# Optimization experiments

Hardware: AMD Instinct MI355X
Metric: run time of the kernel (lower is better)

The kernel has to match this reference:

```python
import jax, jax.numpy as jnp
import numpy as np

N_GAS_NETS = 76  # 29 h2o + 13 o3 + 9 co2 + 3 n2o + 9 ch4 + 13 uniform
N_CHANNELS = 29
N_IN = 2   # (temperature, pressure)
H = 64     # hidden width per n_hidden=[64,64]

# gas index (into composition[0..5]) for each of the 76 stacked nets
COMP_IDX = jnp.asarray(np.repeat(np.arange(6), [29, 13, 9, 3, 9, 13]))

# sparse per-channel combine (hard-coded in the original forward)
H2O_IDX = jnp.asarray([0,1,2,3,4,5,6,3,4,9,10,11,12,13,14,15,16,17,18,19,20,21,22,23,24,25,26,27,28])
O3_CH  = jnp.asarray([0,1,2,17,18,19,20,21,22,25,26,27,28])
CO2_CH = jnp.asarray([0,1,2,5,6,9,10,13,14])
N2O_CH = jnp.asarray([0,1,2])
CH4_CH = jnp.asarray([0,1,2,3,4,7,8,11,12])
U_CH   = jnp.asarray([0,1,2,15,16,17,18,19,20,21,22,27,28])


def setup_inputs() -> dict:
    key = jax.random.key(0)
    ks = jax.random.split(key, 10)
    N = 32768
    t_p = jax.random.normal(ks[0], (N, N_IN), dtype=jnp.float32)
    composition = jax.random.uniform(ks[1], (8, N, 1), dtype=jnp.float32)
    s1 = 1.0 / np.sqrt(N_IN)
    s2 = 1.0 / np.sqrt(H)
    W1 = jax.random.normal(ks[2], (N_GAS_NETS, N_IN, H), dtype=jnp.float32) * s1
    b1 = jnp.zeros((N_GAS_NETS, H), dtype=jnp.float32)
    W2 = jax.random.normal(ks[3], (N_GAS_NETS, H, H), dtype=jnp.float32) * s2
    b2 = jnp.zeros((N_GAS_NETS, H), dtype=jnp.float32)
    Wout = jax.random.normal(ks[4], (N_GAS_NETS, H, 1), dtype=jnp.float32) * s2
    bout = jnp.zeros((N_GAS_NETS, 1), dtype=jnp.float32)
    ke_lw = jax.random.uniform(ks[5], (N_CHANNELS, 1), dtype=jnp.float32)
    ke_iw = jax.random.uniform(ks[6], (N_CHANNELS, 1), dtype=jnp.float32)
    return {"t_p": t_p, "composition": composition, "W1": W1, "b1": b1,
            "W2": W2, "b2": b2, "Wout": Wout, "bout": bout,
            "ke_lw": ke_lw, "ke_iw": ke_iw}


def reference(t_p, composition, W1, b1, W2, b2, Wout, bout, ke_lw, ke_iw):
    # Batched evaluation of all 76 tiny DenseFFN experts on the shared t_p input.
    h = jax.nn.relu(jnp.einsum('ni,gih->gnh', t_p, W1) + b1[:, None, :])   # [76,N,H]
    h = jax.nn.relu(jnp.einsum('gnh,ghk->gnk', h, W2) + b2[:, None, :])    # [76,N,H]
    ke = jax.nn.relu(jnp.einsum('gnh,gho->gno', h, Wout) + bout[:, None, :])  # [76,N,1]

    # tau_gas[gas] = ke * composition[gas_index]
    tau_all = ke * composition[COMP_IDX]  # [76,N,1]
    h2o = tau_all[0:29]
    o3 = tau_all[29:42]
    co2 = tau_all[42:51]
    n2o = tau_all[51:54]
    ch4 = tau_all[54:63]
    u = tau_all[63:76]

    # hard-coded sparse per-channel sum
    tau_gases = h2o[H2O_IDX]                      # [29,N,1]
    tau_gases = tau_gases.at[O3_CH].add(o3)
    tau_gases = tau_gases.at[CO2_CH].add(co2)
    tau_gases = tau_gases.at[N2O_CH].add(n2o)
    tau_gases = tau_gases.at[CH4_CH].add(ch4)
    tau_gases = tau_gases.at[U_CH].add(u)

    tau_lw = ke_lw[:, None, :] * composition[6]   # [29,N,1]
    tau_iw = ke_iw[:, None, :] * composition[7]   # [29,N,1]
    return (tau_gases, tau_lw, tau_iw)
```

## Files before the change

kernel.cpp:

```cpp
#include <hip/hip_runtime.h>

#define NPTS 32768

typedef _Float16 f16;
typedef _Float16 f16x2 __attribute__((ext_vector_type(2)));
typedef _Float16 f16x8 __attribute__((ext_vector_type(8)));
typedef float f32x2 __attribute__((ext_vector_type(2)));
typedef float f32x4 __attribute__((ext_vector_type(4)));
typedef unsigned int u32x4 __attribute__((ext_vector_type(4)));

union U16 { u32x4 u; f32x4 f; f16x2 h2[4]; f16x8 h8; };

static __device__ __forceinline__ f16x2 pk_fma(f16x2 a, f16x2 b, f16x2 c) {
  return __builtin_elementwise_fma(a, b, c);
}
static __device__ __forceinline__ f16x2 pk_relu(f16x2 a) {
  f16x2 z = {(f16)0.f, (f16)0.f};
  return __builtin_elementwise_max(a, z);
}
static __device__ __forceinline__ f16x2 pk_cvt(float a, float b) {
  return __builtin_bit_cast(f16x2, __builtin_amdgcn_cvt_pkrtz(a, b));
}

__device__ const unsigned char G_T[74] = {
  0,0,0,0,0,0,0, 0,0,0,0,0,0,0,0,0,0,0,0,0,0,0,0,0,0,0,0,
  1,1,1,1,1,1,1,1,1,1,1,1,1,
  2,2,2,2,2,2,2,2,2,
  3,3,3,
  4,4,4,4,4,4,4,4,4,
  5,5,5,5,5,5,5,5,5,5,5,5,5
};
__device__ const unsigned char G_C1[74] = {
  0,1,2,3,4,5,6, 9,10,11,12,13,14,15,16,17,18,19,20,21,22,23,24,25,26,27,28,
  0,1,2,17,18,19,20,21,22,25,26,27,28,
  0,1,2,5,6,9,10,13,14,
  0,1,2,
  0,1,2,3,4,7,8,11,12,
  0,1,2,15,16,17,18,19,20,21,22,27,28
};
__device__ const unsigned char G_C2[74] = {
  255,255,255,7,8,255,255, 255,255,255,255,255,255,255,255,255,255,255,255,
  255,255,255,255,255,255,255,255,
  255,255,255,255,255,255,255,255,255,255,255,255,255,
  255,255,255,255,255,255,255,255,255,
  255,255,255,
  255,255,255,255,255,255,255,255,255,
  255,255,255,255,255,255,255,255,255,255,255,255,255
};

#define NSLOT 22

__global__ __launch_bounds__(64) void k0w_pack(
    const float* __restrict__ W1, const float* __restrict__ b1,
    const float* __restrict__ W2, const float* __restrict__ b2,
    const float* __restrict__ Wout, u32x4* __restrict__ pack)
{
  const int gi   = blockIdx.x;
  const int lane = threadIdx.x;
  const int l15  = lane & 15;
  const int quad = lane >> 4;
  const int g    = gi + (gi >= 7 ? 2 : 0);

  const float* W2g = W2 + g * 4096;
  const float* W1g = W1 + g * 128;
  const float* b1g = b1 + g * 64;
  u32x4* dst = pack + gi * NSLOT * 64 + lane;

  #pragma unroll
  for (int mt = 0; mt < 4; ++mt)
    #pragma unroll
    for (int ks = 0; ks < 2; ++ks) {
      U16 u;
      #pragma unroll
      for (int j = 0; j < 4; ++j) {
        const float* s = W2g + (ks * 32 + quad * 8 + 2 * j) * 64 + mt * 16 + l15;
        u.h2[j] = pk_cvt(s[0], s[64]);
      }
      dst[(mt * 2 + ks) * 64] = u.u;
    }
  #pragma unroll
  for (int ks = 0; ks < 2; ++ks) {
    U16 a, b, c;
    #pragma unroll
    for (int j = 0; j < 4; ++j) {
      int h = ks * 32 + quad * 8 + 2 * j;
      a.h2[j] = pk_cvt(W1g[h],      W1g[h + 1]);
      b.h2[j] = pk_cvt(W1g[64 + h], W1g[64 + h + 1]);
      c.h2[j] = pk_cvt(b1g[h],      b1g[h + 1]);
    }
    dst[(8 + ks) * 64]  = a.u;
    dst[(10 + ks) * 64] = b.u;
    dst[(12 + ks) * 64] = c.u;
  }
  #pragma unroll
  for (int mt = 0; mt < 4; ++mt) {
    U16 u, v;
    u.f = *(const f32x4*)(b2   + g * 64 + mt * 16 + quad * 4);
    v.f = *(const f32x4*)(Wout + g * 64 + mt * 16 + quad * 4);
    dst[(14 + mt) * 64] = u.u;
    dst[(18 + mt) * 64] = v.u;
  }
}

__global__ __launch_bounds__(256) void k0_init(
    const float* __restrict__ comp, const float* __restrict__ ke_lw,
    const float* __restrict__ ke_iw, float* __restrict__ out)
{
  const int c = blockIdx.x >> 7;
  const int n = ((blockIdx.x & 127) << 8) + threadIdx.x;
  out[c * NPTS + n] = 0.f;
  out[29 * NPTS + c * NPTS + n] = ke_lw[c] * comp[6 * NPTS + n];
  out[58 * NPTS + c * NPTS + n] = ke_iw[c] * comp[7 * NPTS + n];
}

__global__ __launch_bounds__(256, 2) void k1_mlp(
    const float* __restrict__ t_p, const float* __restrict__ comp,
    const u32x4* __restrict__ pack, const float* __restrict__ bout,
    float* __restrict__ out)
{
  const int lane = threadIdx.x & 63;
  const int l15  = lane & 15;
  const int quad = lane >> 4;
  const int w    = blockIdx.x * 4 + (threadIdx.x >> 6);
  const int gi   = w >> 6;
  const int g    = gi + (gi >= 7 ? 2 : 0);
  const int pb0  = (w & 63) * 512;

  const int t  = G_T[gi];
  const int c1 = G_C1[gi];
  const int c2 = G_C2[gi];

  const bool qb0 = (quad & 1) != 0;
  const bool qb1 = (quad & 2) != 0;

  const u32x4* pksrc = pack + gi * NSLOT * 64 + lane;
  f16x8 afrag[4][2];
  f32x4 b2q[4];
  f32x2 wq2[4][2];
  #pragma unroll
  for (int mt = 0; mt < 4; ++mt) {
    afrag[mt][0] = __builtin_bit_cast(f16x8, pksrc[(mt * 2 + 0) * 64]);
    afrag[mt][1] = __builtin_bit_cast(f16x8, pksrc[(mt * 2 + 1) * 64]);
    b2q[mt] = __builtin_bit_cast(f32x4, pksrc[(14 + mt) * 64]);
    f32x4 wv = __builtin_bit_cast(f32x4, pksrc[(18 + mt) * 64]);
    wq2[mt][0] = f32x2{ wv[0], wv[1] };
    wq2[mt][1] = f32x2{ wv[2], wv[3] };
  }
  U16 w0s[2], w1s[2], b1s[2];
  #pragma unroll
  for (int ks = 0; ks < 2; ++ks) {
    w0s[ks].u = pksrc[(8 + ks) * 64];
    w1s[ks].u = pksrc[(10 + ks) * 64];
    b1s[ks].u = pksrc[(12 + ks) * 64];
  }
  const float bo = bout[g];

  const float2* tp2 = (const float2*)t_p;
  const float* compt = comp + t * NPTS;
  float* out1 = out + c1 * NPTS;
  float* out2 = (c2 == 255) ? nullptr : out + c2 * NPTS;

  for (int pass = 0; pass < 8; ++pass) {
    const int pb = pb0 + pass * 64;

    float2 xv[4];
    #pragma unroll
    for (int pt = 0; pt < 4; ++pt)
      xv[pt] = tp2[pb + pt * 16 + l15];
    const float cv = compt[pb + lane];

    f16x2 x0v[4], x1v[4];
    #pragma unroll
    for (int pt = 0; pt < 4; ++pt) {
      x0v[pt] = pk_cvt(xv[pt].x, xv[pt].x);
      x1v[pt] = pk_cvt(xv[pt].y, xv[pt].y);
    }

    U16 bfrag[2][4];
    #pragma unroll
    for (int ks = 0; ks < 2; ++ks)
      #pragma unroll
      for (int pt = 0; pt < 4; ++pt)
        #pragma unroll
        for (int i = 0; i < 4; ++i)
          bfrag[ks][pt].h2[i] =
              pk_relu(pk_fma(x0v[pt], w0s[ks].h2[i],
                             pk_fma(x1v[pt], w1s[ks].h2[i], b1s[ks].h2[i])));

    f32x2 p2[4];
    #pragma unroll
    for (int pt = 0; pt < 4; ++pt) p2[pt] = f32x2{ 0.f, 0.f };

    #pragma unroll
    for (int mt = 0; mt < 4; ++mt) {
      f32x4 c[4];
      #pragma unroll
      for (int pt = 0; pt < 4; ++pt)
        c[pt] = __builtin_amdgcn_mfma_f32_16x16x32_f16(
            afrag[mt][0], bfrag[0][pt].h8, b2q[mt], 0, 0, 0);
      #pragma unroll
      for (int pt = 0; pt < 4; ++pt)
        c[pt] = __builtin_amdgcn_mfma_f32_16x16x32_f16(
            afrag[mt][1], bfrag[1][pt].h8, c[pt], 0, 0, 0);
      #pragma unroll
      for (int pt = 0; pt < 4; ++pt) {
        f32x2 z = { 0.f, 0.f };
        f32x2 a0 = { c[pt][0], c[pt][1] };
        f32x2 a1 = { c[pt][2], c[pt][3] };
        a0 = __builtin_elementwise_max(a0, z);
        a1 = __builtin_elementwise_max(a1, z);
        p2[pt] = __builtin_elementwise_fma(a0, wq2[mt][0], p2[pt]);
        p2[pt] = __builtin_elementwise_fma(a1, wq2[mt][1], p2[pt]);
      }
    }

    float p[4];
    #pragma unroll
    for (int pt = 0; pt < 4; ++pt) p[pt] = p2[pt][0] + p2[pt][1];

    float u  = qb1 ? (qb0 ? p[3] : p[2]) : (qb0 ? p[1] : p[0]);
    float v  = qb1 ? (qb0 ? p[2] : p[3]) : (qb0 ? p[0] : p[1]);
    float w2 = qb1 ? (qb0 ? p[1] : p[0]) : (qb0 ? p[3] : p[2]);
    float x  = qb1 ? (qb0 ? p[0] : p[1]) : (qb0 ? p[2] : p[3]);
    float s  = u + __shfl_xor(v, 16, 64);
    float tt = w2 + __shfl_xor(x, 16, 64);
    float r  = s + __shfl_xor(tt, 32, 64);

    float tau = fmaxf(r + bo, 0.f) * cv;
    atomicAdd(&out1[pb + lane], tau);
    if (out2) atomicAdd(&out2[pb + lane], tau);
  }
}

extern "C" void kernel_launch(void* const* d_in, const int* in_sizes, int n_in,
                              void* d_out, int out_size, void* d_ws, size_t ws_size,
                              hipStream_t stream)
{
  const float* t_p   = (const float*)d_in[0];
  const float* comp  = (const float*)d_in[1];
  const float* W1    = (const float*)d_in[2];
  const float* b1    = (const float*)d_in[3];
  const float* W2    = (const float*)d_in[4];
  const float* b2    = (const float*)d_in[5];
  const float* Wout  = (const float*)d_in[6];
  const float* bout  = (const float*)d_in[7];
  const float* ke_lw = (const float*)d_in[8];
  const float* ke_iw = (const float*)d_in[9];
  float* out = (float*)d_out;
  u32x4* pack = (u32x4*)d_ws;

  k0w_pack<<<74, 64, 0, stream>>>(W1, b1, W2, b2, Wout, pack);
  k0_init<<<29 * 128, 256, 0, stream>>>(comp, ke_lw, ke_iw, out);
  k1_mlp<<<1184, 256, 0, stream>>>(t_p, comp, pack, bout, out);
}
```

Measured before the change: 113.6 us.

## Balance MLP work across a fixed persistent grid with contiguous unit ranges

Replaces the fixed mapping of one wave per (net, 512-point chunk) with a persistent-style grid of 512 blocks. Each wave takes a contiguous range of 64-point units across nets and reloads net weights whenever it crosses a net boundary. This spreads the 74×512 units evenly over all waves to reduce tail imbalance. It also drops the min-2-blocks launch bound and launches through the cooperative API, falling back to a normal launch on error, which adds host overhead and occasional weight reloads in exchange.

```diff
diff --git a/kernel.cpp b/kernel.cpp
--- a/kernel.cpp
+++ b/kernel.cpp
@@ -113,7 +113,7 @@
   out[58 * NPTS + c * NPTS + n] = ke_iw[c] * comp[7 * NPTS + n];
 }
 
-__global__ __launch_bounds__(256, 2) void k1_mlp(
+__global__ __launch_bounds__(256) void k1_mlp(
     const float* __restrict__ t_p, const float* __restrict__ comp,
     const u32x4* __restrict__ pack, const float* __restrict__ bout,
     float* __restrict__ out)
@@ -121,114 +121,122 @@
   const int lane = threadIdx.x & 63;
   const int l15  = lane & 15;
   const int quad = lane >> 4;
-  const int w    = blockIdx.x * 4 + (threadIdx.x >> 6);
-  const int gi   = w >> 6;
-  const int g    = gi + (gi >= 7 ? 2 : 0);
-  const int pb0  = (w & 63) * 512;
-
-  const int t  = G_T[gi];
-  const int c1 = G_C1[gi];
-  const int c2 = G_C2[gi];
+  const int wv   = blockIdx.x * 4 + (threadIdx.x >> 6);
+  const int NW   = gridDim.x * 4;
+  const int TOT  = 74 * 512;
+
+  int u        = (int)(((long long)wv * TOT) / NW);
+  const int u1 = (int)(((long long)(wv + 1) * TOT) / NW);
 
   const bool qb0 = (quad & 1) != 0;
   const bool qb1 = (quad & 2) != 0;
 
-  const u32x4* pksrc = pack + gi * NSLOT * 64 + lane;
-  f16x8 afrag[4][2];
-  f32x4 b2q[4];
-  f32x2 wq2[4][2];
-  #pragma unroll
-  for (int mt = 0; mt < 4; ++mt) {
-    afrag[mt][0] = __builtin_bit_cast(f16x8, pksrc[(mt * 2 + 0) * 64]);
-    afrag[mt][1] = __builtin_bit_cast(f16x8, pksrc[(mt * 2 + 1) * 64]);
-    b2q[mt] = __builtin_bit_cast(f32x4, pksrc[(14 + mt) * 64]);
-    f32x4 wv = __builtin_bit_cast(f32x4, pksrc[(18 + mt) * 64]);
-    wq2[mt][0] = f32x2{ wv[0], wv[1] };
-    wq2[mt][1] = f32x2{ wv[2], wv[3] };
-  }
-  U16 w0s[2], w1s[2], b1s[2];
-  #pragma unroll
-  for (int ks = 0; ks < 2; ++ks) {
-    w0s[ks].u = pksrc[(8 + ks) * 64];
-    w1s[ks].u = pksrc[(10 + ks) * 64];
-    b1s[ks].u = pksrc[(12 + ks) * 64];
-  }
-  const float bo = bout[g];
-
   const float2* tp2 = (const float2*)t_p;
-  const float* compt = comp + t * NPTS;
-  float* out1 = out + c1 * NPTS;
-  float* out2 = (c2 == 255) ? nullptr : out + c2 * NPTS;
-
-  for (int pass = 0; pass < 8; ++pass) {
-    const int pb = pb0 + pass * 64;
-
-    float2 xv[4];
-    #pragma unroll
-    for (int pt = 0; pt < 4; ++pt)
-      xv[pt] = tp2[pb + pt * 16 + l15];
-    const float cv = compt[pb + lane];
-
-    f16x2 x0v[4], x1v[4];
-    #pragma unroll
-    for (int pt = 0; pt < 4; ++pt) {
-      x0v[pt] = pk_cvt(xv[pt].x, xv[pt].x);
-      x1v[pt] = pk_cvt(xv[pt].y, xv[pt].y);
-    }
-
-    U16 bfrag[2][4];
-    #pragma unroll
-    for (int ks = 0; ks < 2; ++ks)
+
+  while (u < u1) {
+    const int gi   = u >> 9;
+    const int uend = min(u1, (gi + 1) << 9);
+    const int g    = gi + (gi >= 7 ? 2 : 0);
+
+    const int t  = G_T[gi];
+    const int c1 = G_C1[gi];
+    const int c2 = G_C2[gi];
+
+    const u32x4* pksrc = pack + gi * NSLOT * 64 + lane;
+    f16x8 afrag[4][2];
+    f32x4 b2q[4];
+    f32x2 wq2[4][2];
+    #pragma unroll
+    for (int mt = 0; mt < 4; ++mt) {
+      afrag[mt][0] = __builtin_bit_cast(f16x8, pksrc[(mt * 2 + 0) * 64]);
+      afrag[mt][1] = __builtin_bit_cast(f16x8, pksrc[(mt * 2 + 1) * 64]);
+      b2q[mt] = __builtin_bit_cast(f32x4, pksrc[(14 + mt) * 64]);
+      f32x4 wvv = __builtin_bit_cast(f32x4, pksrc[(18 + mt) * 64]);
+      wq2[mt][0] = f32x2{ wvv[0], wvv[1] };
+      wq2[mt][1] = f32x2{ wvv[2], wvv[3] };
+    }
+    U16 w0s[2], w1s[2], b1s[2];
+    #pragma unroll
+    for (int ks = 0; ks < 2; ++ks) {
+      w0s[ks].u = pksrc[(8 + ks) * 64];
+      w1s[ks].u = pksrc[(10 + ks) * 64];
+      b1s[ks].u = pksrc[(12 + ks) * 64];
+    }
+    const float bo = bout[g];
+    const float* compt = comp + t * NPTS;
+    float* out1 = out + c1 * NPTS;
+    float* out2 = (c2 == 255) ? nullptr : out + c2 * NPTS;
+
+    for (; u < uend; ++u) {
+      const int pb = (u & 511) * 64;
+
+      float2 xv[4];
       #pragma unroll
       for (int pt = 0; pt < 4; ++pt)
-        #pragma unroll
-        for (int i = 0; i < 4; ++i)
-          bfrag[ks][pt].h2[i] =
-              pk_relu(pk_fma(x0v[pt], w0s[ks].h2[i],
-                             pk_fma(x1v[pt], w1s[ks].h2[i], b1s[ks].h2[i])));
-
-    f32x2 p2[4];
-    #pragma unroll
-    for (int pt = 0; pt < 4; ++pt) p2[pt] = f32x2{ 0.f, 0.f };
-
-    #pragma unroll
-    for (int mt = 0; mt < 4; ++mt) {
-      f32x4 c[4];
-      #pragma unroll
-      for (int pt = 0; pt < 4; ++pt)
-        c[pt] = __builtin_amdgcn_mfma_f32_16x16x32_f16(
-            afrag[mt][0], bfrag[0][pt].h8, b2q[mt], 0, 0, 0);
-      #pragma unroll
-      for (int pt = 0; pt < 4; ++pt)
-        c[pt] = __builtin_amdgcn_mfma_f32_16x16x32_f16(
-            afrag[mt][1], bfrag[1][pt].h8, c[pt], 0, 0, 0);
+        xv[pt] = tp2[pb + pt * 16 + l15];
+      const float cv = compt[pb + lane];
+
+      f16x2 x0v[4], x1v[4];
       #pragma unroll
       for (int pt = 0; pt < 4; ++pt) {
-        f32x2 z = { 0.f, 0.f };
-        f32x2 a0 = { c[pt][0], c[pt][1] };
-        f32x2 a1 = { c[pt][2], c[pt][3] };
-        a0 = __builtin_elementwise_max(a0, z);
-        a1 = __builtin_elementwise_max(a1, z);
-        p2[pt] = __builtin_elementwise_fma(a0, wq2[mt][0], p2[pt]);
-        p2[pt] = __builtin_elementwise_fma(a1, wq2[mt][1], p2[pt]);
+        x0v[pt] = pk_cvt(xv[pt].x, xv[pt].x);
+        x1v[pt] = pk_cvt(xv[pt].y, xv[pt].y);
       }
-    }
-
-    float p[4];
-    #pragma unroll
-    for (int pt = 0; pt < 4; ++pt) p[pt] = p2[pt][0] + p2[pt][1];
-
-    float u  = qb1 ? (qb0 ? p[3] : p[2]) : (qb0 ? p[1] : p[0]);
-    float v  = qb1 ? (qb0 ? p[2] : p[3]) : (qb0 ? p[0] : p[1]);
-    float w2 = qb1 ? (qb0 ? p[1] : p[0]) : (qb0 ? p[3] : p[2]);
-    float x  = qb1 ? (qb0 ? p[0] : p[1]) : (qb0 ? p[2] : p[3]);
-    float s  = u + __shfl_xor(v, 16, 64);
-    float tt = w2 + __shfl_xor(x, 16, 64);
-    float r  = s + __shfl_xor(tt, 32, 64);
-
-    float tau = fmaxf(r + bo, 0.f) * cv;
-    atomicAdd(&out1[pb + lane], tau);
-    if (out2) atomicAdd(&out2[pb + lane], tau);
+
+      U16 bfrag[2][4];
+      #pragma unroll
+      for (int ks = 0; ks < 2; ++ks)
+        #pragma unroll
+        for (int pt = 0; pt < 4; ++pt)
+          #pragma unroll
+          for (int i = 0; i < 4; ++i)
+            bfrag[ks][pt].h2[i] =
+                pk_relu(pk_fma(x0v[pt], w0s[ks].h2[i],
+                               pk_fma(x1v[pt], w1s[ks].h2[i], b1s[ks].h2[i])));
+
+      f32x2 p2[4];
+      #pragma unroll
+      for (int pt = 0; pt < 4; ++pt) p2[pt] = f32x2{ 0.f, 0.f };
+
+      #pragma unroll
+      for (int mt = 0; mt < 4; ++mt) {
+        f32x4 c[4];
+        #pragma unroll
+        for (int pt = 0; pt < 4; ++pt)
+          c[pt] = __builtin_amdgcn_mfma_f32_16x16x32_f16(
+              afrag[mt][0], bfrag[0][pt].h8, b2q[mt], 0, 0, 0);
+        #pragma unroll
+        for (int pt = 0; pt < 4; ++pt)
+          c[pt] = __builtin_amdgcn_mfma_f32_16x16x32_f16(
+              afrag[mt][1], bfrag[1][pt].h8, c[pt], 0, 0, 0);
+        #pragma unroll
+        for (int pt = 0; pt < 4; ++pt) {
+          f32x2 z = { 0.f, 0.f };
+          f32x2 a0 = { c[pt][0], c[pt][1] };
+          f32x2 a1 = { c[pt][2], c[pt][3] };
+          a0 = __builtin_elementwise_max(a0, z);
+          a1 = __builtin_elementwise_max(a1, z);
+          p2[pt] = __builtin_elementwise_fma(a0, wq2[mt][0], p2[pt]);
+          p2[pt] = __builtin_elementwise_fma(a1, wq2[mt][1], p2[pt]);
+        }
+      }
+
+      float p[4];
+      #pragma unroll
+      for (int pt = 0; pt < 4; ++pt) p[pt] = p2[pt][0] + p2[pt][1];
+
+      float uu = qb1 ? (qb0 ? p[3] : p[2]) : (qb0 ? p[1] : p[0]);
+      float vv = qb1 ? (qb0 ? p[2] : p[3]) : (qb0 ? p[0] : p[1]);
+      float ww = qb1 ? (qb0 ? p[1] : p[0]) : (qb0 ? p[3] : p[2]);
+      float xx = qb1 ? (qb0 ? p[0] : p[1]) : (qb0 ? p[2] : p[3]);
+      float s  = uu + __shfl_xor(vv, 16, 64);
+      float tt = ww + __shfl_xor(xx, 16, 64);
+      float r  = s + __shfl_xor(tt, 32, 64);
+
+      float tau = fmaxf(r + bo, 0.f) * cv;
+      atomicAdd(&out1[pb + lane], tau);
+      if (out2) atomicAdd(&out2[pb + lane], tau);
+    }
   }
 }
 
@@ -251,5 +259,12 @@
 
   k0w_pack<<<74, 64, 0, stream>>>(W1, b1, W2, b2, Wout, pack);
   k0_init<<<29 * 128, 256, 0, stream>>>(comp, ke_lw, ke_iw, out);
-  k1_mlp<<<1184, 256, 0, stream>>>(t_p, comp, pack, bout, out);
-}
+
+  const float* a0 = t_p; const float* a1 = comp;
+  const u32x4* a2 = pack; const float* a3 = bout; float* a4 = out;
+  void* args[] = { (void*)&a0, (void*)&a1, (void*)&a2, (void*)&a3, (void*)&a4 };
+  hipError_t e = hipLaunchCooperativeKernel(
+      reinterpret_cast<const void*>(&k1_mlp), dim3(512), dim3(256), args, 0, stream);
+  if (e != hipSuccess)
+    k1_mlp<<<512, 256, 0, stream>>>(t_p, comp, pack, bout, out);
+}
```

New measurement: 147.4 us. 1.3x slower.

## Restructure MLP kernel per output channel to eliminate atomics and zero-init

Applied to the files above, without the earlier changes.

Each wave now owns one output channel and a 128-point tile. It loops over the gas networks that feed that channel, accumulates tau in registers and does plain stores, instead of one wave per gas network doing atomicAdd into one or two channels. This drops the zero-fill of the gas channels from the init kernel. The output layer now runs as a 16x16x16 f16 MFMA using Wout packed into row 0 of an A fragment, replacing the per-lane FMA and shuffle reduction. The cost is recomputing the h2o networks that feed two channels, uneven work per channel (one to six nets), and extra f16 rounding on the final layer; the pack kernel also carries some odd leftover writes.

```diff
diff --git a/kernel.cpp b/kernel.cpp
--- a/kernel.cpp
+++ b/kernel.cpp
@@ -4,12 +4,14 @@
 
 typedef _Float16 f16;
 typedef _Float16 f16x2 __attribute__((ext_vector_type(2)));
+typedef _Float16 f16x4 __attribute__((ext_vector_type(4)));
 typedef _Float16 f16x8 __attribute__((ext_vector_type(8)));
 typedef float f32x2 __attribute__((ext_vector_type(2)));
 typedef float f32x4 __attribute__((ext_vector_type(4)));
 typedef unsigned int u32x4 __attribute__((ext_vector_type(4)));
 
-union U16 { u32x4 u; f32x4 f; f16x2 h2[4]; f16x8 h8; };
+union U16 { u32x4 u; f32x4 f; f16x2 h2[4]; f16x4 h4[2]; f16x8 h8; };
+union U8h { f16x4 h4; f16x2 h2[2]; };
 
 static __device__ __forceinline__ f16x2 pk_fma(f16x2 a, f16x2 b, f16x2 c) {
   return __builtin_elementwise_fma(a, b, c);
@@ -21,6 +23,12 @@
 static __device__ __forceinline__ f16x2 pk_cvt(float a, float b) {
   return __builtin_bit_cast(f16x2, __builtin_amdgcn_cvt_pkrtz(a, b));
 }
+
+#if __has_builtin(__builtin_amdgcn_mfma_f32_16x16x16f16)
+#define HAVE_MFMA16 1
+#else
+#define HAVE_MFMA16 0
+#endif
 
 __device__ const unsigned char G_T[74] = {
   0,0,0,0,0,0,0, 0,0,0,0,0,0,0,0,0,0,0,0,0,0,0,0,0,0,0,0,
@@ -30,22 +38,16 @@
   4,4,4,4,4,4,4,4,4,
   5,5,5,5,5,5,5,5,5,5,5,5,5
 };
-__device__ const unsigned char G_C1[74] = {
-  0,1,2,3,4,5,6, 9,10,11,12,13,14,15,16,17,18,19,20,21,22,23,24,25,26,27,28,
-  0,1,2,17,18,19,20,21,22,25,26,27,28,
-  0,1,2,5,6,9,10,13,14,
-  0,1,2,
-  0,1,2,3,4,7,8,11,12,
-  0,1,2,15,16,17,18,19,20,21,22,27,28
+__device__ const unsigned char CH_OFF[30] = {
+  0,6,12,18,20,22,24,26,28,30,32,34,36,38,40,42,44,46,49,52,55,58,61,64,
+  65,66,68,70,73,76
 };
-__device__ const unsigned char G_C2[74] = {
-  255,255,255,7,8,255,255, 255,255,255,255,255,255,255,255,255,255,255,255,
-  255,255,255,255,255,255,255,255,
-  255,255,255,255,255,255,255,255,255,255,255,255,255,
-  255,255,255,255,255,255,255,255,255,
-  255,255,255,
-  255,255,255,255,255,255,255,255,255,
-  255,255,255,255,255,255,255,255,255,255,255,255,255
+__device__ const unsigned char CH_GAS[76] = {
+  0,27,40,49,52,61,  1,28,41,50,53,62,  2,29,42,51,54,63,
+  3,55,  4,56,  5,43,  6,44,  3,57,  4,58,  7,45,  8,46,
+  9,59,  10,60,  11,47,  12,48,  13,64,  14,65,
+  15,30,66,  16,31,67,  17,32,68,  18,33,69,  19,34,70,  20,35,71,
+  21,  22,  23,36,  24,37,  25,38,72,  26,39,73
 };
 
 #define NSLOT 22
@@ -98,7 +100,31 @@
     u.f = *(const f32x4*)(b2   + g * 64 + mt * 16 + quad * 4);
     v.f = *(const f32x4*)(Wout + g * 64 + mt * 16 + quad * 4);
     dst[(14 + mt) * 64] = u.u;
-    dst[(18 + mt) * 64] = v.u;
+    dst[(18 + 2 + mt != 0 ? 0 : 0), 0];
+    dst[( (mt < 2 ? 20 : 21) ) * 64] = v.u;
+  }
+  {
+    U16 v0, v1;
+    v0.f = *(const f32x4*)(Wout + g * 64 + 0 * 16 + quad * 4);
+  }
+  {
+    U16 a3a, a3b;
+    #pragma unroll
+    for (int ks = 0; ks < 4; ++ks) {
+      f16x2 lo, hi;
+      if (l15 == 0) {
+        const float* wsrc = Wout + g * 64 + ks * 16 + quad * 4;
+        lo = pk_cvt(wsrc[0], wsrc[1]);
+        hi = pk_cvt(wsrc[2], wsrc[3]);
+      } else {
+        lo = f16x2{(f16)0.f, (f16)0.f};
+        hi = lo;
+      }
+      if (ks < 2) { a3a.h2[ks * 2] = lo; a3a.h2[ks * 2 + 1] = hi; }
+      else        { a3b.h2[(ks - 2) * 2] = lo; a3b.h2[(ks - 2) * 2 + 1] = hi; }
+    }
+    dst[18 * 64] = a3a.u;
+    dst[19 * 64] = a3b.u;
   }
 }
 
@@ -108,12 +134,11 @@
 {
   const int c = blockIdx.x >> 7;
   const int n = ((blockIdx.x & 127) << 8) + threadIdx.x;
-  out[c * NPTS + n] = 0.f;
   out[29 * NPTS + c * NPTS + n] = ke_lw[c] * comp[6 * NPTS + n];
   out[58 * NPTS + c * NPTS + n] = ke_iw[c] * comp[7 * NPTS + n];
 }
 
-__global__ __launch_bounds__(256, 2) void k1_mlp(
+__global__ __launch_bounds__(256) void k1_mlp(
     const float* __restrict__ t_p, const float* __restrict__ comp,
     const u32x4* __restrict__ pack, const float* __restrict__ bout,
     float* __restrict__ out)
@@ -122,113 +147,126 @@
   const int l15  = lane & 15;
   const int quad = lane >> 4;
   const int w    = blockIdx.x * 4 + (threadIdx.x >> 6);
-  const int gi   = w >> 6;
-  const int g    = gi + (gi >= 7 ? 2 : 0);
-  const int pb0  = (w & 63) * 512;
-
-  const int t  = G_T[gi];
-  const int c1 = G_C1[gi];
-  const int c2 = G_C2[gi];
-
+  const int c    = w >> 8;
+  const int pb   = (w & 255) * 128;
+
+  const float2* tp2 = (const float2*)t_p;
+
+  f16x2 x0v[2][4], x1v[2][4];
+  #pragma unroll
+  for (int ps = 0; ps < 2; ++ps)
+    #pragma unroll
+    for (int pt = 0; pt < 4; ++pt) {
+      float2 xv = tp2[pb + ps * 64 + pt * 16 + l15];
+      x0v[ps][pt] = pk_cvt(xv.x, xv.x);
+      x1v[ps][pt] = pk_cvt(xv.y, xv.y);
+    }
+
+  float acc_tau[2][4];
+  #pragma unroll
+  for (int ps = 0; ps < 2; ++ps)
+    #pragma unroll
+    for (int pt = 0; pt < 4; ++pt) acc_tau[ps][pt] = 0.f;
+
+#if !HAVE_MFMA16
   const bool qb0 = (quad & 1) != 0;
   const bool qb1 = (quad & 2) != 0;
-
-  const u32x4* pksrc = pack + gi * NSLOT * 64 + lane;
-  f16x8 afrag[4][2];
-  f32x4 b2q[4];
-  f32x2 wq2[4][2];
-  #pragma unroll
-  for (int mt = 0; mt < 4; ++mt) {
-    afrag[mt][0] = __builtin_bit_cast(f16x8, pksrc[(mt * 2 + 0) * 64]);
-    afrag[mt][1] = __builtin_bit_cast(f16x8, pksrc[(mt * 2 + 1) * 64]);
-    b2q[mt] = __builtin_bit_cast(f32x4, pksrc[(14 + mt) * 64]);
-    f32x4 wv = __builtin_bit_cast(f32x4, pksrc[(18 + mt) * 64]);
-    wq2[mt][0] = f32x2{ wv[0], wv[1] };
-    wq2[mt][1] = f32x2{ wv[2], wv[3] };
-  }
-  U16 w0s[2], w1s[2], b1s[2];
-  #pragma unroll
-  for (int ks = 0; ks < 2; ++ks) {
-    w0s[ks].u = pksrc[(8 + ks) * 64];
-    w1s[ks].u = pksrc[(10 + ks) * 64];
-    b1s[ks].u = pksrc[(12 + ks) * 64];
-  }
-  const float bo = bout[g];
-
-  const float2* tp2 = (const float2*)t_p;
-  const float* compt = comp + t * NPTS;
-  float* out1 = out + c1 * NPTS;
-  float* out2 = (c2 == 255) ? nullptr : out + c2 * NPTS;
-
-  for (int pass = 0; pass < 8; ++pass) {
-    const int pb = pb0 + pass * 64;
-
-    float2 xv[4];
-    #pragma unroll
-    for (int pt = 0; pt < 4; ++pt)
-      xv[pt] = tp2[pb + pt * 16 + l15];
-    const float cv = compt[pb + lane];
-
-    f16x2 x0v[4], x1v[4];
-    #pragma unroll
-    for (int pt = 0; pt < 4; ++pt) {
-      x0v[pt] = pk_cvt(xv[pt].x, xv[pt].x);
-      x1v[pt] = pk_cvt(xv[pt].y, xv[pt].y);
-    }
-
-    U16 bfrag[2][4];
-    #pragma unroll
-    for (int ks = 0; ks < 2; ++ks)
+#endif
+
+  const int i0 = CH_OFF[c], i1 = CH_OFF[c + 1];
+  for (int idx = i0; idx < i1; ++idx) {
+    const int gi = CH_GAS[idx];
+    const int t  = G_T[gi];
+    const int g  = gi + (gi >= 7 ? 2 : 0);
+
+    const u32x4* pksrc = pack + gi * NSLOT * 64 + lane;
+    f16x8 afrag[4][2];
+    f32x4 b2q[4];
+    #pragma unroll
+    for (int mt = 0; mt < 4; ++mt) {
+      afrag[mt][0] = __builtin_bit_cast(f16x8, pksrc[(mt * 2 + 0) * 64]);
+      afrag[mt][1] = __builtin_bit_cast(f16x8, pksrc[(mt * 2 + 1) * 64]);
+      b2q[mt] = __builtin_bit_cast(f32x4, pksrc[(14 + mt) * 64]);
+    }
+    U16 w0s[2], w1s[2], b1s[2];
+    #pragma unroll
+    for (int ks = 0; ks < 2; ++ks) {
+      w0s[ks].u = pksrc[(8 + ks) * 64];
+      w1s[ks].u = pksrc[(10 + ks) * 64];
+      b1s[ks].u = pksrc[(12 + ks) * 64];
+    }
+#if HAVE_MFMA16
+    U16 a3a, a3b;
+    a3a.u = pksrc[18 * 64];
+    a3b.u = pksrc[19 * 64];
+    f16x4 a3[4] = { a3a.h4[0], a3a.h4[1], a3b.h4[0], a3b.h4[1] };
+#else
+    f32x2 wq2[4][2];
+    #pragma unroll
+    for (int mt = 0; mt < 4; ++mt) {
+      wq2[mt][0] = f32x2{0.f, 0.f};
+      wq2[mt][1] = f32x2{0.f, 0.f};
+    }
+#endif
+    const float bo = bout[g];
+    const float* compt = comp + t * NPTS;
+
+    #pragma unroll
+    for (int ps = 0; ps < 2; ++ps) {
+      U16 bfrag[2][4];
+      #pragma unroll
+      for (int ks = 0; ks < 2; ++ks)
+        #pragma unroll
+        for (int pt = 0; pt < 4; ++pt)
+          #pragma unroll
+          for (int i = 0; i < 4; ++i)
+            bfrag[ks][pt].h2[i] =
+                pk_relu(pk_fma(x0v[ps][pt], w0s[ks].h2[i],
+                               pk_fma(x1v[ps][pt], w1s[ks].h2[i], b1s[ks].h2[i])));
+
+      #pragma unroll
+      for (int pt = 0; pt < 4; ++pt) {
+        f32x4 a4[4];
+        #pragma unroll
+        for (int mt = 0; mt < 4; ++mt) {
+          f32x4 c0 = __builtin_amdgcn_mfma_f32_16x16x32_f16(
+              afrag[mt][0], bfrag[0][pt].h8, b2q[mt], 0, 0, 0);
+          a4[mt] = __builtin_amdgcn_mfma_f32_16x16x32_f16(
+              afrag[mt][1], bfrag[1][pt].h8, c0, 0, 0, 0);
+        }
+
+#if HAVE_MFMA16
+        f32x4 d3 = { 0.f, 0.f, 0.f, 0.f };
+        #pragma unroll
+        for (int ks = 0; ks < 4; ++ks) {
+          f32x4 z = { 0.f, 0.f, 0.f, 0.f };
+          f32x4 r4 = __builtin_elementwise_max(a4[ks], z);
+          U8h b3;
+          b3.h2[0] = pk_cvt(r4[0], r4[1]);
+          b3.h2[1] = pk_cvt(r4[2], r4[3]);
+          d3 = __builtin_amdgcn_mfma_f32_16x16x16f16(a3[ks], b3.h4, d3, 0, 0, 0);
+        }
+        float cvv = compt[pb + ps * 64 + pt * 16 + l15];
+        float tau = fmaxf(d3[0] + bo, 0.f) * cvv;
+        acc_tau[ps][pt] += tau;
+#else
+        float p = 0.f;
+        #pragma unroll
+        for (int mt = 0; mt < 4; ++mt)
+          #pragma unroll
+          for (int r = 0; r < 4; ++r) p += fmaxf(a4[mt][r], 0.f);
+        acc_tau[ps][pt] += p;
+#endif
+      }
+    }
+  }
+
+  if (quad == 0) {
+    #pragma unroll
+    for (int ps = 0; ps < 2; ++ps)
       #pragma unroll
       for (int pt = 0; pt < 4; ++pt)
-        #pragma unroll
-        for (int i = 0; i < 4; ++i)
-          bfrag[ks][pt].h2[i] =
-              pk_relu(pk_fma(x0v[pt], w0s[ks].h2[i],
-                             pk_fma(x1v[pt], w1s[ks].h2[i], b1s[ks].h2[i])));
-
-    f32x2 p2[4];
-    #pragma unroll
-    for (int pt = 0; pt < 4; ++pt) p2[pt] = f32x2{ 0.f, 0.f };
-
-    #pragma unroll
-    for (int mt = 0; mt < 4; ++mt) {
-      f32x4 c[4];
-      #pragma unroll
-      for (int pt = 0; pt < 4; ++pt)
-        c[pt] = __builtin_amdgcn_mfma_f32_16x16x32_f16(
-            afrag[mt][0], bfrag[0][pt].h8, b2q[mt], 0, 0, 0);
-      #pragma unroll
-      for (int pt = 0; pt < 4; ++pt)
-        c[pt] = __builtin_amdgcn_mfma_f32_16x16x32_f16(
-            afrag[mt][1], bfrag[1][pt].h8, c[pt], 0, 0, 0);
-      #pragma unroll
-      for (int pt = 0; pt < 4; ++pt) {
-        f32x2 z = { 0.f, 0.f };
-        f32x2 a0 = { c[pt][0], c[pt][1] };
-        f32x2 a1 = { c[pt][2], c[pt][3] };
-        a0 = __builtin_elementwise_max(a0, z);
-        a1 = __builtin_elementwise_max(a1, z);
-        p2[pt] = __builtin_elementwise_fma(a0, wq2[mt][0], p2[pt]);
-        p2[pt] = __builtin_elementwise_fma(a1, wq2[mt][1], p2[pt]);
-      }
-    }
-
-    float p[4];
-    #pragma unroll
-    for (int pt = 0; pt < 4; ++pt) p[pt] = p2[pt][0] + p2[pt][1];
-
-    float u  = qb1 ? (qb0 ? p[3] : p[2]) : (qb0 ? p[1] : p[0]);
-    float v  = qb1 ? (qb0 ? p[2] : p[3]) : (qb0 ? p[0] : p[1]);
-    float w2 = qb1 ? (qb0 ? p[1] : p[0]) : (qb0 ? p[3] : p[2]);
-    float x  = qb1 ? (qb0 ? p[0] : p[1]) : (qb0 ? p[2] : p[3]);
-    float s  = u + __shfl_xor(v, 16, 64);
-    float tt = w2 + __shfl_xor(x, 16, 64);
-    float r  = s + __shfl_xor(tt, 32, 64);
-
-    float tau = fmaxf(r + bo, 0.f) * cv;
-    atomicAdd(&out1[pb + lane], tau);
-    if (out2) atomicAdd(&out2[pb + lane], tau);
+        out[c * NPTS + pb + ps * 64 + pt * 16 + l15] = acc_tau[ps][pt];
   }
 }
 
@@ -251,5 +289,5 @@
 
   k0w_pack<<<74, 64, 0, stream>>>(W1, b1, W2, b2, Wout, pack);
   k0_init<<<29 * 128, 256, 0, stream>>>(comp, ke_lw, ke_iw, out);
-  k1_mlp<<<1184, 256, 0, stream>>>(t_p, comp, pack, bout, out);
-}
+  k1_mlp<<<1856, 256, 0, stream>>>(t_p, comp, pack, bout, out);
+}
```

After: 156.1 us. 37.3% more time.
